# Optimization experiments

Measured on AMD Instinct MI355X. Metric: run time of the kernel, lower is better.

## Reference

```python
import math
import jax, jax.numpy as jnp
import numpy as np

INPUT_DIM = 1024
OUTPUT_DIM = 1024
DEGREE = 8
EPS = 1.0


def setup_inputs() -> dict:
    key = jax.random.key(0)
    k1, k2 = jax.random.split(key)
    x = jax.random.normal(k1, (8192, INPUT_DIM), dtype=jnp.float32)
    std = 1.0 / (INPUT_DIM * (DEGREE + 1))
    hermite_coeffs = std * jax.random.normal(k2, (INPUT_DIM, OUTPUT_DIM, DEGREE + 1), dtype=jnp.float32)
    return {"x": x, "hermite_coeffs": hermite_coeffs}


def _hermite_basis(x):
    # x: [B, I] squashed input; returns [B, I, DEGREE+1] Hermite-function basis.
    pi_q = math.pi ** (-0.25)
    gauss = jnp.exp(-0.5 * x * x)
    h0 = pi_q * gauss
    hs = [h0]
    if DEGREE > 0:
        hs.append(math.sqrt(2.0) * pi_q * x * gauss)
    for i in range(2, DEGREE + 1):
        hs.append(math.sqrt(2.0 / i) * x * hs[i - 1] - math.sqrt((i - 1) / i) * hs[i - 2])
    return jnp.stack(hs, axis=-1)


def reference(x, hermite_coeffs):
    x = x.reshape(-1, INPUT_DIM)
    x = jnp.tanh(x) * (math.sqrt(2 * DEGREE + 1) + EPS)
    hermite = _hermite_basis(x)  # [B, I, D+1]
    y = jnp.einsum('bid,iod->bo', hermite, hermite_coeffs)
    return y.reshape(-1, OUTPUT_DIM)
```

## Files before the change

kernel.cpp:

```cpp
#include <hip/hip_runtime.h>

#define MDIM 8192
#define IDIM 1024
#define ODIM 1024
#define D1   9
#define KDIM (IDIM * D1)

typedef _Float16 half8   __attribute__((ext_vector_type(8)));
typedef _Float16 half2v  __attribute__((ext_vector_type(2)));
typedef float    float4v __attribute__((ext_vector_type(4)));

#define BSCALE 256.0f
#define INV_BSCALE (1.0f / 256.0f)
#define USCALE 5.123105625617661f
#define H0C 0.7511255444649425f
#define SQRT2 1.4142135623730951f

__device__ __forceinline__ void hermite9(float xv, float h[D1]) {
    float ax = fabsf(xv);
    float t  = __expf(-2.0f * ax);
    float th = (1.0f - t) / (1.0f + t);
    th = copysignf(th, xv);
    float u = th * USCALE;
    float g = __expf(-0.5f * u * u);
    h[0] = H0C * g;
    h[1] = SQRT2 * H0C * u * g;
    const float c1[D1] = {0.f, 0.f, 1.0f, 0.8164965809277260f, 0.7071067811865476f,
                          0.6324555320336759f, 0.5773502691896258f, 0.5345224838248488f, 0.5f};
    const float c2[D1] = {0.f, 0.f, 0.7071067811865476f, 0.8164965809277260f, 0.8660254037844386f,
                          0.8944271909999159f, 0.9128709291752769f, 0.9258200997725514f, 0.9354143466934853f};
#pragma unroll
    for (int d = 2; d < D1; ++d) h[d] = c1[d] * u * h[d - 1] - c2[d] * h[d - 2];
}

__global__ __launch_bounds__(256) void prep_all(const float* __restrict__ C,
                                                const float* __restrict__ x,
                                                _Float16* __restrict__ Bt,
                                                _Float16* __restrict__ U,
                                                _Float16* __restrict__ H0) {
    __shared__ float lds[288 * 33];
    const int t = threadIdx.x;
    if (blockIdx.x < 1024) {
        const int ti = blockIdx.x & 31;
        const int to = blockIdx.x >> 5;
        const float* base = C + (size_t)ti * 32 * 9216 + (size_t)to * 32 * 9;
#pragma unroll
        for (int j = 0; j < 36; ++j) {
            int f   = t + 256 * j;
            int row = f / 288;
            int col = f - row * 288;
            lds[col * 33 + row] = base[(size_t)row * 9216 + col];
        }
        __syncthreads();
        _Float16* bb = Bt + (size_t)to * 32 * KDIM + ti * 32;
#pragma unroll
        for (int j = 0; j < 5; ++j) {
            int s = t + 256 * j;
            if (s < 1152) {
                int i8  = s & 3;
                int odp = s >> 2;
                int ol  = odp / 9;
                int d   = odp - ol * 9;
                half8 vv;
#pragma unroll
                for (int e = 0; e < 8; ++e)
                    vv[e] = (_Float16)(lds[odp * 33 + i8 * 8 + e] * BSCALE);
                *(half8*)(bb + (size_t)ol * KDIM + d * IDIM + i8 * 8) = vv;
            }
        }
    } else {
        size_t tt = (size_t)(blockIdx.x - 1024) * 256 + t;
        const float4* xp = (const float4*)(x + tt * 8);
        float4 a0 = xp[0], a1 = xp[1];
        float xv[8] = {a0.x, a0.y, a0.z, a0.w, a1.x, a1.y, a1.z, a1.w};
        half8 uu, hh;
#pragma unroll
        for (int e = 0; e < 8; ++e) {
            float v  = xv[e];
            float t2 = __expf(-2.0f * fabsf(v));
            float th = (1.0f - t2) / (1.0f + t2);
            float u  = copysignf(th, v) * USCALE;
            float g  = __expf(-0.5f * u * u);
            uu[e] = (_Float16)u;
            hh[e] = (_Float16)(H0C * g);
        }
        *(half8*)(U  + tt * 8) = uu;
        *(half8*)(H0 + tt * 8) = hh;
    }
}

__global__ __launch_bounds__(256, 2) void gemm_fused6(
    const _Float16* __restrict__ U,
    const _Float16* __restrict__ H0,
    const _Float16* __restrict__ Bt,
    float* __restrict__ out)
{
    const int tid = threadIdx.x;
    const int w = tid >> 6;
    const int l = tid & 63;
    const int bn = blockIdx.x;
    const int bm = blockIdx.y;

    __shared__ _Float16 Bs[3][128 * 64];

    const int lrow8 = l >> 3;
    const int kgrp  = (l & 7) ^ lrow8;
    const _Float16* Bg = Bt + ((size_t)(bn * 128 + w * 8 + lrow8) * KDIM + kgrp * 8);

    const int q   = l >> 4;
    const int m16 = l & 15;
    const int s3  = m16 & 7;
    const int wm  = w >> 1, wn = w & 1;

    const size_t ubase = ((size_t)(bm * 128 + wm * 64 + m16)) << 10;

    constexpr float c1a[D1] = {0.f, 0.f, 1.0f, 0.8164965809277260f, 0.7071067811865476f,
                               0.6324555320336759f, 0.5773502691896258f, 0.5345224838248488f, 0.5f};
    constexpr float c2a[D1] = {0.f, 0.f, 0.7071067811865476f, 0.8164965809277260f, 0.8660254037844386f,
                               0.8944271909999159f, 0.9128709291752769f, 0.9258200997725514f, 0.9354143466934853f};

    half8 u8[8], hA8[8], hB8[8];

    auto loadUH = [&](int ib) {
        const int ibo = ib * 64;
#pragma unroll
        for (int i16 = 0; i16 < 4; ++i16)
#pragma unroll
            for (int ko = 0; ko < 2; ++ko) {
                const size_t off = ubase + ((size_t)(i16 * 16) << 10) + ibo + (q + 4 * ko) * 8;
                u8 [i16 * 2 + ko] = *(const half8*)(U  + off);
                hA8[i16 * 2 + ko] = *(const half8*)(H0 + off);
            }
    };

    auto dmaB = [&](int nkoff, int nbuf) {
#pragma unroll
        for (int rr = 0; rr < 4; ++rr)
            __builtin_amdgcn_global_load_lds(
                (const __attribute__((address_space(1))) void*)(Bg + (size_t)(rr * 32) * KDIM + nkoff),
                (__attribute__((address_space(3))) void*)((char*)&Bs[nbuf][0] + (rr * 4 + w) * 1024),
                16, 0, 0);
    };

    float4v acc[4][4] = {};

    loadUH(0);
    dmaB(0, 0);
    dmaB(IDIM, 1);
    asm volatile("s_waitcnt vmcnt(4)" ::: "memory");
    __builtin_amdgcn_s_barrier();
    asm volatile("" ::: "memory");

    auto window = [&](int ib, int d, bool do_uh, bool do_dma, int waitN, bool do_sync) {
        const int cbuf = d % 3;

        if (do_uh) loadUH(ib + 1);

        const _Float16 s2 = (_Float16)SQRT2;
        const _Float16 c1 = (_Float16)c1a[d + 1 <= 8 ? d + 1 : 8];
        const _Float16 c2 = (_Float16)c2a[d + 1 <= 8 ? d + 1 : 8];
        const half8 s2v = {s2, s2, s2, s2, s2, s2, s2, s2};
        const half8 c1v = {c1, c1, c1, c1, c1, c1, c1, c1};
        const half8 c2v = {c2, c2, c2, c2, c2, c2, c2, c2};

        __builtin_amdgcn_s_setprio(1);
#pragma unroll
        for (int ko = 0; ko < 2; ++ko) {
            const int slot = (q + 4 * ko) ^ s3;
            half8 bf[4];
#pragma unroll
            for (int j = 0; j < 4; ++j)
                bf[j] = *(const half8*)&Bs[cbuf][(wn * 64 + j * 16 + m16) * 64 + slot * 8];
#pragma unroll
            for (int i = 0; i < 4; ++i) {
                const int p = i * 2 + ko;
                half8 af = (d == 0) ? hA8[p] : hB8[p];
#pragma unroll
                for (int j = 0; j < 4; ++j)
                    acc[i][j] = __builtin_amdgcn_mfma_f32_16x16x32_f16(af, bf[j], acc[i][j], 0, 0, 0);
                if (d == 0) {
                    hB8[p] = s2v * u8[p] * hA8[p];
                } else if (d <= 7) {
                    half8 tt = u8[p] * hB8[p];
                    half8 ht = c1v * tt - c2v * hA8[p];
                    hA8[p] = hB8[p];
                    hB8[p] = ht;
                }
            }
        }
        __builtin_amdgcn_s_setprio(0);

        if (do_dma) {
            const int nkoff = (d <= 6) ? ((d + 2) * IDIM + ib * 64)
                                       : ((d - 7) * IDIM + ib * 64 + 64);
            dmaB(nkoff, (d + 2) % 3);
        }

        if (do_sync) {
            if (waitN == 4) asm volatile("s_waitcnt vmcnt(4) lgkmcnt(0)" ::: "memory");
            else            asm volatile("s_waitcnt vmcnt(0) lgkmcnt(0)" ::: "memory");
            __builtin_amdgcn_s_barrier();
            asm volatile("" ::: "memory");
        }
    };

    for (int ib = 0; ib < 15; ++ib) {
#pragma unroll
        for (int d = 0; d < D1; ++d)
            window(ib, d,  (d == 8),  true,  4,  true);
    }
    {
#pragma unroll
        for (int d = 0; d < 7; ++d)
            window(15, d, false, true, 4, true);
        window(15, 7, false, false, 0, true);
        window(15, 8, false, false, 0, false);
    }

#pragma unroll
    for (int i = 0; i < 4; ++i) {
        int row = bm * 128 + wm * 64 + i * 16 + q * 4;
#pragma unroll
        for (int j = 0; j < 4; ++j) {
            int col = bn * 128 + wn * 64 + j * 16 + m16;
            float* op = out + (size_t)row * ODIM + col;
#pragma unroll
            for (int r2 = 0; r2 < 4; ++r2)
                op[(size_t)r2 * ODIM] = acc[i][j][r2] * INV_BSCALE;
        }
    }
}

__global__ void naive_kernel(const float* __restrict__ x, const float* __restrict__ C,
                             float* __restrict__ out) {
    __shared__ float hb[IDIM * D1];
    int b = blockIdx.x;
    int tid = threadIdx.x;
    for (int i = tid; i < IDIM; i += 256) {
        float h[D1];
        hermite9(x[(size_t)b * IDIM + i], h);
#pragma unroll
        for (int d = 0; d < D1; ++d) hb[i * D1 + d] = h[d];
    }
    __syncthreads();
    for (int o = tid; o < ODIM; o += 256) {
        float acc = 0.f;
        for (int i = 0; i < IDIM; ++i) {
            const float* cp = C + ((size_t)i * ODIM + o) * D1;
            const float* hp = hb + i * D1;
#pragma unroll
            for (int d = 0; d < D1; ++d) acc += hp[d] * cp[d];
        }
        out[(size_t)b * ODIM + o] = acc;
    }
}

extern "C" void kernel_launch(void* const* d_in, const int* in_sizes, int n_in,
                              void* d_out, int out_size, void* d_ws, size_t ws_size,
                              hipStream_t stream) {
    const float* x      = (const float*)d_in[0];
    const float* coeffs = (const float*)d_in[1];
    float* out = (float*)d_out;

    const size_t bt_bytes = (size_t)ODIM * KDIM * sizeof(_Float16);
    const size_t u_bytes  = (size_t)MDIM * IDIM * sizeof(_Float16);

    if (ws_size >= bt_bytes + 2 * u_bytes) {
        _Float16* Bt = (_Float16*)d_ws;
        _Float16* Uv = (_Float16*)((char*)d_ws + bt_bytes);
        _Float16* H0 = (_Float16*)((char*)d_ws + bt_bytes + u_bytes);
        hipLaunchKernelGGL(prep_all, dim3(1024 + 4096), dim3(256), 0, stream,
                           coeffs, x, Bt, Uv, H0);
        hipLaunchKernelGGL(gemm_fused6, dim3(8, 64), dim3(256), 0, stream, Uv, H0, Bt, out);
    } else {
        hipLaunchKernelGGL(naive_kernel, dim3(MDIM), dim3(256), 0, stream, x, coeffs, out);
    }
}
```

Baseline: 273.3 us.

## Deepen B pipeline to four LDS buffers with register double-buffered fragment prefetch

Grows the shared-memory B ring from three to four stages, so the global-to-LDS DMA runs three windows ahead. B fragments for the next window are read from LDS into a second register set before the current window's MFMAs issue, so LDS read latency overlaps with matrix math. The Hermite recurrence update moves out of the MFMA loop into a separate pass after the MFMAs. The cost is more LDS per block (64KB vs 48KB) and more VGPRs for the doubled fragment registers, which may hurt occupancy at two blocks per CU, along with more complex wait and barrier bookkeeping.

```diff
diff --git a/kernel.cpp b/kernel.cpp
--- a/kernel.cpp
+++ b/kernel.cpp
@@ -7,7 +7,6 @@
 #define KDIM (IDIM * D1)
 
 typedef _Float16 half8   __attribute__((ext_vector_type(8)));
-typedef _Float16 half2v  __attribute__((ext_vector_type(2)));
 typedef float    float4v __attribute__((ext_vector_type(4)));
 
 #define BSCALE 256.0f
@@ -89,7 +88,7 @@
     }
 }
 
-__global__ __launch_bounds__(256, 2) void gemm_fused6(
+__global__ __launch_bounds__(256, 2) void gemm_fused8(
     const _Float16* __restrict__ U,
     const _Float16* __restrict__ H0,
     const _Float16* __restrict__ Bt,
@@ -101,7 +100,7 @@
     const int bn = blockIdx.x;
     const int bm = blockIdx.y;
 
-    __shared__ _Float16 Bs[3][128 * 64];
+    __shared__ _Float16 Bs[4][128 * 64];
 
     const int lrow8 = l >> 3;
     const int kgrp  = (l & 7) ^ lrow8;
@@ -120,6 +119,7 @@
                                0.8944271909999159f, 0.9128709291752769f, 0.9258200997725514f, 0.9354143466934853f};
 
     half8 u8[8], hA8[8], hB8[8];
+    half8 bfA[8], bfB[8];
 
     auto loadUH = [&](int ib) {
         const int ibo = ib * 64;
@@ -131,6 +131,7 @@
                 u8 [i16 * 2 + ko] = *(const half8*)(U  + off);
                 hA8[i16 * 2 + ko] = *(const half8*)(H0 + off);
             }
+        asm volatile("" ::: "memory");
     };
 
     auto dmaB = [&](int nkoff, int nbuf) {
@@ -142,79 +143,111 @@
                 16, 0, 0);
     };
 
+    auto prefB = [&](int buf, half8 (&dst)[8]) {
+#pragma unroll
+        for (int ko = 0; ko < 2; ++ko) {
+            const int slot = (q + 4 * ko) ^ s3;
+#pragma unroll
+            for (int j = 0; j < 4; ++j)
+                dst[ko * 4 + j] = *(const half8*)&Bs[buf][(wn * 64 + j * 16 + m16) * 64 + slot * 8];
+        }
+    };
+
     float4v acc[4][4] = {};
 
     loadUH(0);
     dmaB(0, 0);
     dmaB(IDIM, 1);
+    dmaB(2 * IDIM, 2);
     asm volatile("s_waitcnt vmcnt(4)" ::: "memory");
     __builtin_amdgcn_s_barrier();
     asm volatile("" ::: "memory");
-
-    auto window = [&](int ib, int d, bool do_uh, bool do_dma, int waitN, bool do_sync) {
-        const int cbuf = d % 3;
+    prefB(0, bfA);
+    asm volatile("" ::: "memory");
+
+    auto window = [&](int ib, int d, bool do_uh, bool do_dma, int waitN,
+                      bool do_pref, bool do_sync,
+                      half8 (&bfC)[8], half8 (&bfN)[8]) {
+        if (do_pref) prefB((ib * 9 + d + 1) & 3, bfN);
+        asm volatile("" ::: "memory");
 
         if (do_uh) loadUH(ib + 1);
 
-        const _Float16 s2 = (_Float16)SQRT2;
-        const _Float16 c1 = (_Float16)c1a[d + 1 <= 8 ? d + 1 : 8];
-        const _Float16 c2 = (_Float16)c2a[d + 1 <= 8 ? d + 1 : 8];
-        const half8 s2v = {s2, s2, s2, s2, s2, s2, s2, s2};
-        const half8 c1v = {c1, c1, c1, c1, c1, c1, c1, c1};
-        const half8 c2v = {c2, c2, c2, c2, c2, c2, c2, c2};
-
         __builtin_amdgcn_s_setprio(1);
 #pragma unroll
-        for (int ko = 0; ko < 2; ++ko) {
-            const int slot = (q + 4 * ko) ^ s3;
-            half8 bf[4];
-#pragma unroll
-            for (int j = 0; j < 4; ++j)
-                bf[j] = *(const half8*)&Bs[cbuf][(wn * 64 + j * 16 + m16) * 64 + slot * 8];
+        for (int ko = 0; ko < 2; ++ko)
 #pragma unroll
             for (int i = 0; i < 4; ++i) {
                 const int p = i * 2 + ko;
                 half8 af = (d == 0) ? hA8[p] : hB8[p];
 #pragma unroll
                 for (int j = 0; j < 4; ++j)
-                    acc[i][j] = __builtin_amdgcn_mfma_f32_16x16x32_f16(af, bf[j], acc[i][j], 0, 0, 0);
-                if (d == 0) {
-                    hB8[p] = s2v * u8[p] * hA8[p];
-                } else if (d <= 7) {
-                    half8 tt = u8[p] * hB8[p];
-                    half8 ht = c1v * tt - c2v * hA8[p];
-                    hA8[p] = hB8[p];
-                    hB8[p] = ht;
-                }
+                    acc[i][j] = __builtin_amdgcn_mfma_f32_16x16x32_f16(af, bfC[ko * 4 + j], acc[i][j], 0, 0, 0);
             }
-        }
         __builtin_amdgcn_s_setprio(0);
 
+        if (d == 0) {
+            const _Float16 s2 = (_Float16)SQRT2;
+            half8 s2v = {s2, s2, s2, s2, s2, s2, s2, s2};
+#pragma unroll
+            for (int p = 0; p < 8; ++p) hB8[p] = s2v * u8[p] * hA8[p];
+        } else if (d <= 7) {
+            const _Float16 c1 = (_Float16)c1a[d + 1];
+            const _Float16 c2 = (_Float16)c2a[d + 1];
+            half8 c1v = {c1, c1, c1, c1, c1, c1, c1, c1};
+            half8 c2v = {c2, c2, c2, c2, c2, c2, c2, c2};
+#pragma unroll
+            for (int p = 0; p < 8; ++p) {
+                half8 tt = u8[p] * hB8[p];
+                half8 ht = c1v * tt - c2v * hA8[p];
+                hA8[p] = hB8[p];
+                hB8[p] = ht;
+            }
+        }
+
         if (do_dma) {
-            const int nkoff = (d <= 6) ? ((d + 2) * IDIM + ib * 64)
-                                       : ((d - 7) * IDIM + ib * 64 + 64);
-            dmaB(nkoff, (d + 2) % 3);
-        }
-
+            int dd = d + 3, iib = ib;
+            if (dd >= 9) { dd -= 9; iib += 1; }
+            dmaB(dd * IDIM + iib * 64, (ib * 9 + d + 3) & 3);
+        }
+
+        if (waitN == 4)      asm volatile("s_waitcnt vmcnt(4)" ::: "memory");
+        else if (waitN == 0) asm volatile("s_waitcnt vmcnt(0)" ::: "memory");
         if (do_sync) {
-            if (waitN == 4) asm volatile("s_waitcnt vmcnt(4) lgkmcnt(0)" ::: "memory");
-            else            asm volatile("s_waitcnt vmcnt(0) lgkmcnt(0)" ::: "memory");
             __builtin_amdgcn_s_barrier();
             asm volatile("" ::: "memory");
         }
     };
 
-    for (int ib = 0; ib < 15; ++ib) {
-#pragma unroll
-        for (int d = 0; d < D1; ++d)
-            window(ib, d,  (d == 8),  true,  4,  true);
-    }
-    {
-#pragma unroll
-        for (int d = 0; d < 7; ++d)
-            window(15, d, false, true, 4, true);
-        window(15, 7, false, false, 0, true);
-        window(15, 8, false, false, 0, false);
+    for (int ib2 = 0; ib2 < 7; ++ib2) {
+        const int ib0 = ib2 * 2;
+#pragma unroll
+        for (int d18 = 0; d18 < 18; ++d18) {
+            const int ibl = ib0 + (d18 / 9);
+            const int d   = d18 % 9;
+            if ((d18 & 1) == 0)
+                window(ibl, d, d == 8, true, 4, true, true, bfA, bfB);
+            else
+                window(ibl, d, d == 8, true, 4, true, true, bfB, bfA);
+        }
+    }
+#pragma unroll
+    for (int d = 0; d < 9; ++d) {
+        if ((d & 1) == 0)
+            window(14, d, d == 8, true, 4, true, true, bfA, bfB);
+        else
+            window(14, d, d == 8, true, 4, true, true, bfB, bfA);
+    }
+#pragma unroll
+    for (int d = 0; d < 9; ++d) {
+        const bool dma  = (d <= 5);
+        const int  wN   = (d <= 5) ? 4 : (d == 6 ? 0 : -1);
+        const bool pref = (d <= 7);
+        const bool sync = (d <= 7);
+        if ((d & 1) == 0)
+            window(15, d, false, dma, wN, pref, sync, bfB, bfA);
+        else
+            window(15, d, false, dma, wN, pref, sync, bfA, bfB);
     }
 
 #pragma unroll
@@ -271,7 +304,7 @@
         _Float16* H0 = (_Float16*)((char*)d_ws + bt_bytes + u_bytes);
         hipLaunchKernelGGL(prep_all, dim3(1024 + 4096), dim3(256), 0, stream,
                            coeffs, x, Bt, Uv, H0);
-        hipLaunchKernelGGL(gemm_fused6, dim3(8, 64), dim3(256), 0, stream, Uv, H0, Bt, out);
+        hipLaunchKernelGGL(gemm_fused8, dim3(8, 64), dim3(256), 0, stream, Uv, H0, Bt, out);
     } else {
         hipLaunchKernelGGL(naive_kernel, dim3(MDIM), dim3(256), 0, stream, x, coeffs, out);
     }
```

Result: slower. 310.2 us (+13.5%).

## Process two K-windows per barrier with four-buffer LDS double-pair pipeline

Applied to the files above, without the earlier changes.

Restructures the GEMM main loop from one 64-wide K window per barrier with triple buffering to pairs of windows per barrier, using four LDS buffers so the DMA writes one pair while the MFMAs consume the other. The Hermite recurrence is moved out of the MFMA loop into a separate step after each window, and U/H0 prefetch is placed between windows. The aim is to halve the number of barriers and waitcnt stalls. In exchange, LDS use grows from 48 KB to 64 KB per block, which may limit occupancy at two blocks per CU, and each barrier now waits on vmcnt(0), leaving less DMA overlap.

```diff
diff --git a/kernel.cpp b/kernel.cpp
--- a/kernel.cpp
+++ b/kernel.cpp
@@ -7,7 +7,6 @@
 #define KDIM (IDIM * D1)
 
 typedef _Float16 half8   __attribute__((ext_vector_type(8)));
-typedef _Float16 half2v  __attribute__((ext_vector_type(2)));
 typedef float    float4v __attribute__((ext_vector_type(4)));
 
 #define BSCALE 256.0f
@@ -89,7 +88,7 @@
     }
 }
 
-__global__ __launch_bounds__(256, 2) void gemm_fused6(
+__global__ __launch_bounds__(256, 2) void gemm_fused9(
     const _Float16* __restrict__ U,
     const _Float16* __restrict__ H0,
     const _Float16* __restrict__ Bt,
@@ -101,7 +100,7 @@
     const int bn = blockIdx.x;
     const int bm = blockIdx.y;
 
-    __shared__ _Float16 Bs[3][128 * 64];
+    __shared__ _Float16 Bs[4][128 * 64];
 
     const int lrow8 = l >> 3;
     const int kgrp  = (l & 7) ^ lrow8;
@@ -120,6 +119,8 @@
                                0.8944271909999159f, 0.9128709291752769f, 0.9258200997725514f, 0.9354143466934853f};
 
     half8 u8[8], hA8[8], hB8[8];
+    float4v acc[4][4] = {};
+    int bA = 0;
 
     auto loadUH = [&](int ib) {
         const int ibo = ib * 64;
@@ -131,6 +132,7 @@
                 u8 [i16 * 2 + ko] = *(const half8*)(U  + off);
                 hA8[i16 * 2 + ko] = *(const half8*)(H0 + off);
             }
+        asm volatile("" ::: "memory");
     };
 
     auto dmaB = [&](int nkoff, int nbuf) {
@@ -142,79 +144,90 @@
                 16, 0, 0);
     };
 
-    float4v acc[4][4] = {};
+    auto wnd = [&](int buf, bool useH0) {
+        const _Float16* bp = &Bs[0][0] + (size_t)buf * (128 * 64);
+        __builtin_amdgcn_s_setprio(1);
+#pragma unroll
+        for (int ko = 0; ko < 2; ++ko) {
+            const int slot = (q + 4 * ko) ^ s3;
+            half8 bf[4];
+#pragma unroll
+            for (int j = 0; j < 4; ++j)
+                bf[j] = *(const half8*)(bp + (wn * 64 + j * 16 + m16) * 64 + slot * 8);
+#pragma unroll
+            for (int i = 0; i < 4; ++i) {
+                half8 af = useH0 ? hA8[i * 2 + ko] : hB8[i * 2 + ko];
+#pragma unroll
+                for (int j = 0; j < 4; ++j)
+                    acc[i][j] = __builtin_amdgcn_mfma_f32_16x16x32_f16(af, bf[j], acc[i][j], 0, 0, 0);
+            }
+        }
+        __builtin_amdgcn_s_setprio(0);
+    };
+
+    auto recur = [&](int d) {
+        if (d == 0) {
+            const _Float16 s2 = (_Float16)SQRT2;
+            half8 s2v = {s2, s2, s2, s2, s2, s2, s2, s2};
+#pragma unroll
+            for (int p = 0; p < 8; ++p) hB8[p] = s2v * u8[p] * hA8[p];
+        } else if (d <= 7) {
+            const _Float16 c1 = (_Float16)c1a[d + 1];
+            const _Float16 c2 = (_Float16)c2a[d + 1];
+            half8 c1v = {c1, c1, c1, c1, c1, c1, c1, c1};
+            half8 c2v = {c2, c2, c2, c2, c2, c2, c2, c2};
+#pragma unroll
+            for (int p = 0; p < 8; ++p) {
+                half8 tt = u8[p] * hB8[p];
+                half8 ht = c1v * tt - c2v * hA8[p];
+                hA8[p] = hB8[p];
+                hB8[p] = ht;
+            }
+        }
+    };
 
     loadUH(0);
     dmaB(0, 0);
     dmaB(IDIM, 1);
-    asm volatile("s_waitcnt vmcnt(4)" ::: "memory");
+    asm volatile("" ::: "memory");
+    asm volatile("s_waitcnt vmcnt(0) lgkmcnt(0)" ::: "memory");
     __builtin_amdgcn_s_barrier();
     asm volatile("" ::: "memory");
 
-    auto window = [&](int ib, int d, bool do_uh, bool do_dma, int waitN, bool do_sync) {
-        const int cbuf = d % 3;
-
-        if (do_uh) loadUH(ib + 1);
-
-        const _Float16 s2 = (_Float16)SQRT2;
-        const _Float16 c1 = (_Float16)c1a[d + 1 <= 8 ? d + 1 : 8];
-        const _Float16 c2 = (_Float16)c2a[d + 1 <= 8 ? d + 1 : 8];
-        const half8 s2v = {s2, s2, s2, s2, s2, s2, s2, s2};
-        const half8 c1v = {c1, c1, c1, c1, c1, c1, c1, c1};
-        const half8 c2v = {c2, c2, c2, c2, c2, c2, c2, c2};
-
-        __builtin_amdgcn_s_setprio(1);
-#pragma unroll
-        for (int ko = 0; ko < 2; ++ko) {
-            const int slot = (q + 4 * ko) ^ s3;
-            half8 bf[4];
-#pragma unroll
-            for (int j = 0; j < 4; ++j)
-                bf[j] = *(const half8*)&Bs[cbuf][(wn * 64 + j * 16 + m16) * 64 + slot * 8];
-#pragma unroll
-            for (int i = 0; i < 4; ++i) {
-                const int p = i * 2 + ko;
-                half8 af = (d == 0) ? hA8[p] : hB8[p];
-#pragma unroll
-                for (int j = 0; j < 4; ++j)
-                    acc[i][j] = __builtin_amdgcn_mfma_f32_16x16x32_f16(af, bf[j], acc[i][j], 0, 0, 0);
-                if (d == 0) {
-                    hB8[p] = s2v * u8[p] * hA8[p];
-                } else if (d <= 7) {
-                    half8 tt = u8[p] * hB8[p];
-                    half8 ht = c1v * tt - c2v * hA8[p];
-                    hA8[p] = hB8[p];
-                    hB8[p] = ht;
-                }
-            }
-        }
-        __builtin_amdgcn_s_setprio(0);
-
-        if (do_dma) {
-            const int nkoff = (d <= 6) ? ((d + 2) * IDIM + ib * 64)
-                                       : ((d - 7) * IDIM + ib * 64 + 64);
-            dmaB(nkoff, (d + 2) % 3);
-        }
-
-        if (do_sync) {
-            if (waitN == 4) asm volatile("s_waitcnt vmcnt(4) lgkmcnt(0)" ::: "memory");
-            else            asm volatile("s_waitcnt vmcnt(0) lgkmcnt(0)" ::: "memory");
+    auto region = [&](int uhIb, int uhMode, bool dma, int kA, int kB,
+                      int dA, int dB, bool endSync) {
+        if (uhMode == 1) loadUH(uhIb);
+        if (dma) {
+            dmaB(kA, bA ^ 2);
+            dmaB(kB, (bA ^ 2) + 1);
+            asm volatile("" ::: "memory");
+        }
+        wnd(bA, dA == 0);
+        recur(dA);
+        if (uhMode == 2) loadUH(uhIb);
+        wnd(bA + 1, dB == 0);
+        recur(dB);
+        if (endSync) {
+            asm volatile("s_waitcnt vmcnt(0) lgkmcnt(0)" ::: "memory");
             __builtin_amdgcn_s_barrier();
             asm volatile("" ::: "memory");
         }
-    };
-
-    for (int ib = 0; ib < 15; ++ib) {
-#pragma unroll
-        for (int d = 0; d < D1; ++d)
-            window(ib, d,  (d == 8),  true,  4,  true);
-    }
-    {
-#pragma unroll
-        for (int d = 0; d < 7; ++d)
-            window(15, d, false, true, 4, true);
-        window(15, 7, false, false, 0, true);
-        window(15, 8, false, false, 0, false);
+        bA ^= 2;
+    };
+
+    for (int p = 0; p < 8; ++p) {
+        const int ib0 = 2 * p;
+        const int o0 = ib0 * 64, o1 = o0 + 64, o2 = o0 + 128;
+        const bool more = (p < 7);
+        region(0,     0, true, 2*IDIM + o0, 3*IDIM + o0, 0, 1, true);
+        region(0,     0, true, 4*IDIM + o0, 5*IDIM + o0, 2, 3, true);
+        region(0,     0, true, 6*IDIM + o0, 7*IDIM + o0, 4, 5, true);
+        region(0,     0, true, 8*IDIM + o0, o1,          6, 7, true);
+        region(ib0+1, 1, true, 1*IDIM + o1, 2*IDIM + o1, 8, 0, true);
+        region(0,     0, true, 3*IDIM + o1, 4*IDIM + o1, 1, 2, true);
+        region(0,     0, true, 5*IDIM + o1, 6*IDIM + o1, 3, 4, true);
+        region(0,     0, true, 7*IDIM + o1, 8*IDIM + o1, 5, 6, true);
+        region(ib0+2, more ? 2 : 0, more, o2, 1*IDIM + o2, 7, 8, more);
     }
 
 #pragma unroll
@@ -271,7 +284,7 @@
         _Float16* H0 = (_Float16*)((char*)d_ws + bt_bytes + u_bytes);
         hipLaunchKernelGGL(prep_all, dim3(1024 + 4096), dim3(256), 0, stream,
                            coeffs, x, Bt, Uv, H0);
-        hipLaunchKernelGGL(gemm_fused6, dim3(8, 64), dim3(256), 0, stream, Uv, H0, Bt, out);
+        hipLaunchKernelGGL(gemm_fused9, dim3(8, 64), dim3(256), 0, stream, Uv, H0, Bt, out);
     } else {
         hipLaunchKernelGGL(naive_kernel, dim3(MDIM), dim3(256), 0, stream, x, coeffs, out);
     }
```

Result: slower. 287.0 us (+5.0%).
